# Kernel tuning notes

Hardware: AMD Instinct MI355X
Metric: run time of the kernel (lower is better)

The kernel has to match this reference:

```python
import jax, jax.numpy as jnp
import numpy as np

B, C, H, W = 4, 64, 256, 256
HEADS, WS = 2, 8
HID = int(C * 2.66)  # 170


def _layernorm(x, w, b):
    # Restormer per-pixel channel LayerNorm over C of BCHW, biased var, eps=1e-5
    mu = x.mean(axis=1, keepdims=True)
    var = x.var(axis=1, keepdims=True)
    xn = (x - mu) / jnp.sqrt(var + 1e-5)
    return xn * w[None, :, None, None] + b[None, :, None, None]


def _conv1x1(x, w, b=None):
    y = jnp.einsum('oc,bchw->bohw', w, x)
    if b is not None:
        y = y + b[None, :, None, None]
    return y


def _dwconv3(x, w):
    # depthwise 3x3, zero padding ('zeros' padding_mode)
    return jax.lax.conv_general_dilated(
        x, w, window_strides=(1, 1), padding='SAME',
        dimension_numbers=('NCHW', 'OIHW', 'NCHW'),
        feature_group_count=x.shape[1])


def _l2norm(x, eps=1e-12):
    n = jnp.sqrt(jnp.sum(x * x, axis=-1, keepdims=True))
    return x / jnp.maximum(n, eps)


def _attention(xn, qkv_w, qkv_dw_w, temperature, proj_w, proj_b):
    qkv = _dwconv3(_conv1x1(xn, qkv_w), qkv_dw_w)  # [B, 3C, H, W]
    h1, w1 = H // WS, W // WS
    c = C // HEADS
    # 'b (z head c) (h1 h) (w1 w) -> z (b h1 w1) head c (h w)'
    t = qkv.reshape(B, 3, HEADS, c, h1, WS, w1, WS)
    t = t.transpose(1, 0, 4, 6, 2, 3, 5, 7).reshape(3, B * h1 * w1, HEADS, c, WS * WS)
    q, k, v = t[0], t[1], t[2]
    q = _l2norm(q)
    k = _l2norm(k)
    attn = jnp.einsum('nhcd,nhed->nhce', q, k) * temperature  # [n, heads, c, c]
    attn = jax.nn.softmax(attn, axis=-1)
    out = jnp.einsum('nhce,nhed->nhcd', attn, v)
    # '(b h1 w1) head c (h w) -> b (head c) (h1 h) (w1 w)'
    out = out.reshape(B, h1, w1, HEADS, c, WS, WS)
    out = out.transpose(0, 3, 4, 1, 5, 2, 6).reshape(B, C, H, W)
    return _conv1x1(out, proj_w, proj_b)


def _ffn(xn, pin_w, dw_w, pout_w):
    y = _dwconv3(_conv1x1(xn, pin_w), dw_w)  # [B, 2*HID, H, W]
    y1, y2 = y[:, :HID], y[:, HID:]
    y = jax.nn.gelu(y1, approximate=False) * y2
    return _conv1x1(y, pout_w)


def setup_inputs() -> dict:
    key = jax.random.key(0)
    ks = jax.random.split(key, 8)
    s = 0.02
    return {
        'x': jax.random.normal(ks[0], (B, C, H, W), jnp.float32),
        'ln1_w': jnp.ones((C,), jnp.float32),
        'ln1_b': jnp.zeros((C,), jnp.float32),
        'qkv_w': jax.random.normal(ks[1], (3 * C, C), jnp.float32) * s,
        'qkv_dw_w': jax.random.normal(ks[2], (3 * C, 1, 3, 3), jnp.float32) * s,
        'temperature': jnp.ones((HEADS, 1, 1), jnp.float32) / np.float32(np.sqrt(C)),
        'proj_w': jax.random.normal(ks[3], (C, C), jnp.float32) * s,
        'proj_b': jnp.zeros((C,), jnp.float32),
        'ln2_w': jnp.ones((C,), jnp.float32),
        'ln2_b': jnp.zeros((C,), jnp.float32),
        'pin_w': jax.random.normal(ks[4], (2 * HID, C), jnp.float32) * s,
        'dw_w': jax.random.normal(ks[5], (2 * HID, 1, 3, 3), jnp.float32) * s,
        'pout_w': jax.random.normal(ks[6], (C, HID), jnp.float32) * s,
    }


def reference(x, ln1_w, ln1_b, qkv_w, qkv_dw_w, temperature, proj_w, proj_b,
              ln2_w, ln2_b, pin_w, dw_w, pout_w):
    x = x + _attention(_layernorm(x, ln1_w, ln1_b), qkv_w, qkv_dw_w,
                       temperature, proj_w, proj_b)
    x = x + _ffn(_layernorm(x, ln2_w, ln2_b), pin_w, dw_w, pout_w)
    return x
```

## Files before the change

kernel.cpp:

```cpp
#include <hip/hip_runtime.h>
#include <math.h>

typedef __attribute__((ext_vector_type(8))) short short8;
typedef __attribute__((ext_vector_type(4))) float f32x4;

#define HID 170
#define PLANE 65536

__device__ __forceinline__ unsigned short f2bf(float f) {
  unsigned u = __float_as_uint(f);
  u += 0x7FFFu + ((u >> 16) & 1u);
  return (unsigned short)(u >> 16);
}
__device__ __forceinline__ float bf2f(unsigned short h) {
  return __uint_as_float(((unsigned)h) << 16);
}
__device__ __forceinline__ float bf2f_lo(unsigned v) { return __uint_as_float(v << 16); }
__device__ __forceinline__ float bf2f_hi(unsigned v) { return __uint_as_float(v & 0xFFFF0000u); }
__device__ __forceinline__ unsigned pack2bf(float a, float b) {
  return (unsigned)f2bf(a) | ((unsigned)f2bf(b) << 16);
}
__device__ __forceinline__ f32x4 mfma16(short8 a, short8 b, f32x4 c) {
  return __builtin_amdgcn_mfma_f32_16x16x32_bf16(a, b, c, 0, 0, 0);
}

__global__ void prepack_kernel(const float* __restrict__ qkv_w, const float* __restrict__ proj_w,
                               const float* __restrict__ pin_w, const float* __restrict__ pout_w,
                               short* __restrict__ pq, short* __restrict__ pp,
                               short* __restrict__ pi, short* __restrict__ po) {
  int idx = blockIdx.x * 256 + threadIdx.x;
  if (idx < 12288) {
    int j = idx & 7, ln = (idx >> 3) & 63, ks = (idx >> 9) & 1, mt = idx >> 10;
    int row = mt * 16 + (ln & 15), k = ks * 32 + (ln >> 4) * 8 + j;
    pq[idx] = (short)f2bf(qkv_w[row * 64 + k]);
  }
  if (idx < 4096) {
    int j = idx & 7, ln = (idx >> 3) & 63, ks = (idx >> 9) & 1, mt = idx >> 10;
    int row = mt * 16 + (ln & 15), k = ks * 32 + (ln >> 4) * 8 + j;
    pp[idx] = (short)f2bf(proj_w[row * 64 + k]);
  }
  if (idx < 22528) {
    int j = idx & 7, ln = (idx >> 3) & 63, ks = (idx >> 9) & 1, mt = idx >> 10;
    int r = mt * 16 + (ln & 15), k = ks * 32 + (ln >> 4) * 8 + j;
    int c = r >> 7; if (c > 2) c = 2;
    int loc = r - c * 128;
    int half = (c < 2) ? 64 : 48, limit = (c < 2) ? 64 : 42;
    float v = 0.f;
    if (loc < half) { int i = loc; if (i < limit) v = pin_w[(c * 64 + i) * 64 + k]; }
    else { int i = loc - half; if (i < limit) v = pin_w[(HID + c * 64 + i) * 64 + k]; }
    pi[idx] = (short)f2bf(v);
  }
  if (idx < 12288) {
    int j = idx & 7, ln = (idx >> 3) & 63, ks = (idx >> 9) % 6, mt = idx / 3072;
    int o = mt * 16 + (ln & 15), k = ks * 32 + (ln >> 4) * 8 + j;
    float v = (k < 170) ? pout_w[o * 170 + k] : 0.f;
    po[idx] = (short)f2bf(v);
  }
}

__global__ __launch_bounds__(256) void ln_kernel(
    const float* __restrict__ src, const float* __restrict__ w,
    const float* __restrict__ bia, unsigned short* __restrict__ dst) {
  __shared__ float xT[64 * 65];
  const int t = threadIdx.x;
  const int g = blockIdx.x << 6;
  const int bi = g >> 16;
  const int hw = g & 65535;
  {
    int c = t >> 2, q = t & 3;
    const float* sp = src + ((size_t)(bi * 64 + c) << 16) + hw + q * 16;
    float4 v0 = *(const float4*)(sp);
    float4 v1 = *(const float4*)(sp + 4);
    float4 v2 = *(const float4*)(sp + 8);
    float4 v3 = *(const float4*)(sp + 12);
    float* row = xT + c * 65 + q * 16;
    row[0] = v0.x; row[1] = v0.y; row[2] = v0.z; row[3] = v0.w;
    row[4] = v1.x; row[5] = v1.y; row[6] = v1.z; row[7] = v1.w;
    row[8] = v2.x; row[9] = v2.y; row[10] = v2.z; row[11] = v2.w;
    row[12] = v3.x; row[13] = v3.y; row[14] = v3.z; row[15] = v3.w;
  }
  __syncthreads();
  const int p = t >> 2, q = t & 3;
  float s = 0.f, s2 = 0.f;
  float vv[16];
#pragma unroll
  for (int i = 0; i < 16; ++i) {
    float v = xT[(q * 16 + i) * 65 + p];
    vv[i] = v; s += v; s2 += v * v;
  }
  s += __shfl_xor(s, 1); s2 += __shfl_xor(s2, 1);
  s += __shfl_xor(s, 2); s2 += __shfl_xor(s2, 2);
  float mu = s * (1.f / 64.f);
  float var = s2 * (1.f / 64.f) - mu * mu;
  float rstd = rsqrtf(var + 1e-5f);
  short8 o0, o1;
#pragma unroll
  for (int i = 0; i < 8; ++i) {
    o0[i] = (short)f2bf((vv[i] - mu) * rstd * w[q * 16 + i] + bia[q * 16 + i]);
    o1[i] = (short)f2bf((vv[8 + i] - mu) * rstd * w[q * 16 + 8 + i] + bia[q * 16 + 8 + i]);
  }
  unsigned short* dp = dst + (size_t)(g + p) * 64 + q * 16;
  *(short8*)dp = o0;
  *(short8*)(dp + 8) = o1;
}

#define A_QK    0
#define A_VT    18432
#define A_XN    27648
#define A_QKVT  41984
#define A_SCL   41984
#define A_PP    42496
#define A_PB    50944
#define A_OW    56064
#define A_TOT   65280

__global__ __launch_bounds__(512) void attn_kernel(
    const unsigned short* __restrict__ xn1, const float* __restrict__ x,
    const float* __restrict__ qkv_dw, const float* __restrict__ temp,
    const float* __restrict__ proj_b,
    const short* __restrict__ pk_qkv, const short* __restrict__ pk_proj,
    float* __restrict__ x1out) {
  __shared__ __align__(16) char smem[A_TOT];
  short* qk      = (short*)(smem + A_QK);
  short* vt      = (short*)(smem + A_VT);
  short* xn      = (short*)(smem + A_XN);
  unsigned* qkvt = (unsigned*)(smem + A_QKVT);
  float* scl     = (float*)(smem + A_SCL);
  float* pP      = (float*)(smem + A_PP);
  short* pB      = (short*)(smem + A_PB);
  short* ow      = (short*)(smem + A_OW);

  const int tid = threadIdx.x;
  const int lane = tid & 63;
  const int wid = tid >> 6;
  const int l15 = lane & 15, q4 = lane >> 4;
  const int blk = blockIdx.x;
  const int b = blk >> 10, wy = (blk >> 5) & 31, wx = blk & 31;
  const int gy0 = wy * 8 - 1, gx0 = wx * 8 - 1;
  const size_t nb = (size_t)b << 16;

  for (int u = tid; u < 896; u += 512) {
    int p = u >> 3, q = u & 7;
    short8 v = {0, 0, 0, 0, 0, 0, 0, 0};
    if (p < 100) {
      int py = p / 10, px = p - py * 10;
      int gy = gy0 + py, gx = gx0 + px;
      if ((unsigned)gy < 256u && (unsigned)gx < 256u)
        v = *(const short8*)(xn1 + ((nb + gy * 256 + gx) << 6) + q * 8);
    }
    *(short8*)(xn + p * 64 + ((q ^ (p & 7)) << 3)) = v;
  }
  __syncthreads();

  for (int cc = 0; cc < 2; ++cc) {
    for (int f = wid; f < 42; f += 8) {
      int mt = f / 7, nt = f - mt * 7;
      int gmt = cc * 6 + mt;
      f32x4 acc = {0.f, 0.f, 0.f, 0.f};
#pragma unroll
      for (int ks = 0; ks < 2; ++ks) {
        short8 a = *(const short8*)(pk_qkv + ((gmt * 2 + ks) * 64 + lane) * 8);
        int pos0 = nt * 16 + l15;
        short8 bb = *(const short8*)(xn + pos0 * 64 + (((ks * 4 + q4) ^ (pos0 & 7)) << 3));
        acc = mfma16(a, bb, acc);
      }
      int pos = nt * 16 + l15;
      if (pos < 100) {
        int pb = mt * 8 + q4 * 2;
        qkvt[pb * 102 + pos]       = pack2bf(acc[0], acc[1]);
        qkvt[(pb + 1) * 102 + pos] = pack2bf(acc[2], acc[3]);
      }
    }
    __syncthreads();
    if (tid < 384) {
      int p = tid >> 3, r = tid & 7;
      int gp = cc * 48 + p;
      const float* w0 = qkv_dw + gp * 18;
      const float* w1 = w0 + 9;
      const unsigned* src = qkvt + p * 102;
      float accA[8], accB[8];
#pragma unroll
      for (int j = 0; j < 8; ++j) { accA[j] = 0.f; accB[j] = 0.f; }
#pragma unroll
      for (int t = 0; t < 3; ++t) {
        const unsigned* rp = src + (r + t) * 10;
        uint2 u0 = *(const uint2*)(rp);
        uint2 u1 = *(const uint2*)(rp + 2);
        uint2 u2 = *(const uint2*)(rp + 4);
        uint2 u3 = *(const uint2*)(rp + 6);
        uint2 u4 = *(const uint2*)(rp + 8);
        float lo[10], hi[10];
        lo[0] = bf2f_lo(u0.x); hi[0] = bf2f_hi(u0.x);
        lo[1] = bf2f_lo(u0.y); hi[1] = bf2f_hi(u0.y);
        lo[2] = bf2f_lo(u1.x); hi[2] = bf2f_hi(u1.x);
        lo[3] = bf2f_lo(u1.y); hi[3] = bf2f_hi(u1.y);
        lo[4] = bf2f_lo(u2.x); hi[4] = bf2f_hi(u2.x);
        lo[5] = bf2f_lo(u2.y); hi[5] = bf2f_hi(u2.y);
        lo[6] = bf2f_lo(u3.x); hi[6] = bf2f_hi(u3.x);
        lo[7] = bf2f_lo(u3.y); hi[7] = bf2f_hi(u3.y);
        lo[8] = bf2f_lo(u4.x); hi[8] = bf2f_hi(u4.x);
        lo[9] = bf2f_lo(u4.y); hi[9] = bf2f_hi(u4.y);
        float wa0 = w0[t * 3], wa1 = w0[t * 3 + 1], wa2 = w0[t * 3 + 2];
        float wb0 = w1[t * 3], wb1 = w1[t * 3 + 1], wb2 = w1[t * 3 + 2];
#pragma unroll
        for (int px = 0; px < 8; ++px) {
          accA[px] = fmaf(wa0, lo[px], fmaf(wa1, lo[px + 1], fmaf(wa2, lo[px + 2], accA[px])));
          accB[px] = fmaf(wb0, hi[px], fmaf(wb1, hi[px + 1], fmaf(wb2, hi[px + 2], accB[px])));
        }
      }
      if (gp < 64) {
        short8 sa, sb;
#pragma unroll
        for (int j = 0; j < 8; ++j) { sa[j] = (short)f2bf(accA[j]); sb[j] = (short)f2bf(accB[j]); }
        *(short8*)(qk + (2 * gp) * 72 + r * 8) = sa;
        *(short8*)(qk + (2 * gp + 1) * 72 + r * 8) = sb;
      } else {
        int vb = (gp - 64) * 2;
#pragma unroll
        for (int px = 0; px < 8; ++px)
          *(unsigned*)(vt + (r * 8 + px) * 72 + vb) = pack2bf(accA[px], accB[px]);
      }
    }
    __syncthreads();
  }

  {
    int row = tid >> 2, qq = tid & 3;
    const short* r = qk + row * 72 + qq * 16;
    short8 v0 = *(const short8*)(r);
    short8 v1 = *(const short8*)(r + 8);
    float s = 0.f;
#pragma unroll
    for (int j = 0; j < 8; ++j) {
      float f0 = bf2f((unsigned short)v0[j]); s = fmaf(f0, f0, s);
      float f1 = bf2f((unsigned short)v1[j]); s = fmaf(f1, f1, s);
    }
    s += __shfl_xor(s, 1);
    s += __shfl_xor(s, 2);
    if (qq == 0) scl[row] = 1.f / fmaxf(sqrtf(s), 1e-12f);
  }
  __syncthreads();

  {
    int h = wid >> 2, mt = (wid >> 1) & 1, nt = wid & 1;
    int arow = h * 32 + mt * 16;
    int brow = 64 + h * 32 + nt * 16;
    f32x4 acc = {0.f, 0.f, 0.f, 0.f};
#pragma unroll
    for (int ks = 0; ks < 2; ++ks) {
      short8 a = *(const short8*)(qk + (arow + l15) * 72 + ks * 32 + q4 * 8);
      short8 bb = *(const short8*)(qk + (brow + l15) * 72 + ks * 32 + q4 * 8);
      acc = mfma16(a, bb, acc);
    }
    float tf = temp[h];
    int e = nt * 16 + l15;
    float se = scl[64 + h * 32 + e] * tf;
    int cqb = h * 32 + mt * 16 + q4 * 4;
#pragma unroll
    for (int j = 0; j < 4; ++j)
      pP[(cqb + j) * 33 + e] = acc[j] * scl[cqb + j] * se;
  }
  __syncthreads();

  {
    int row = tid >> 3, l = tid & 7;
    const float* rp = pP + row * 33 + l * 4;
    float e0 = rp[0], e1 = rp[1], e2 = rp[2], e3 = rp[3];
    float m = fmaxf(fmaxf(e0, e1), fmaxf(e2, e3));
    m = fmaxf(m, __shfl_xor(m, 1));
    m = fmaxf(m, __shfl_xor(m, 2));
    m = fmaxf(m, __shfl_xor(m, 4));
    float x0 = __expf(e0 - m), x1v = __expf(e1 - m);
    float x2 = __expf(e2 - m), x3 = __expf(e3 - m);
    float s = x0 + x1v + x2 + x3;
    s += __shfl_xor(s, 1);
    s += __shfl_xor(s, 2);
    s += __shfl_xor(s, 4);
    float inv = 1.f / s;
    unsigned* dp = (unsigned*)(pB + row * 40 + l * 4);
    dp[0] = pack2bf(x0 * inv, x1v * inv);
    dp[1] = pack2bf(x2 * inv, x3 * inv);
  }
  __syncthreads();

#pragma unroll
  for (int r = 0; r < 2; ++r) {
    int f = wid + r * 8;
    int h = f >> 3, mt = (f >> 2) & 1, nt = f & 3;
    short8 a = *(const short8*)(pB + (h * 32 + mt * 16 + l15) * 40 + q4 * 8);
    short8 bb = *(const short8*)(vt + (nt * 16 + l15) * 72 + h * 32 + q4 * 8);
    f32x4 acc = {0.f, 0.f, 0.f, 0.f};
    acc = mfma16(a, bb, acc);
    int d = nt * 16 + l15;
    int chb = h * 32 + mt * 16 + q4 * 4;
    unsigned* dp = (unsigned*)(ow + d * 72 + chb);
    dp[0] = pack2bf(acc[0], acc[1]);
    dp[1] = pack2bf(acc[2], acc[3]);
  }
  __syncthreads();

#pragma unroll
  for (int r = 0; r < 2; ++r) {
    int f = wid + r * 8;
    int mt = f >> 2, nt = f & 3;
    f32x4 acc = {0.f, 0.f, 0.f, 0.f};
#pragma unroll
    for (int ks = 0; ks < 2; ++ks) {
      short8 a = *(const short8*)(pk_proj + ((mt * 2 + ks) * 64 + lane) * 8);
      short8 bb = *(const short8*)(ow + (nt * 16 + l15) * 72 + ks * 32 + q4 * 8);
      acc = mfma16(a, bb, acc);
    }
    int pos = nt * 16 + l15;
    int gy = wy * 8 + (pos >> 3), gx = wx * 8 + (pos & 7);
    int ob = mt * 16 + q4 * 4;
#pragma unroll
    for (int j = 0; j < 4; ++j) {
      int o = ob + j;
      size_t gp = (size_t)(b * 64 + o) * PLANE + gy * 256 + gx;
      x1out[gp] = acc[j] + proj_b[o] + x[gp];
    }
  }
}

#define F_XN  0
#define F_Y12 14336
#define F_G   40448
#define F_TOT 49664

__global__ __launch_bounds__(512) void ffn_kernel(
    const unsigned short* __restrict__ xn2,
    const float* __restrict__ dw_w,
    const short* __restrict__ pk_pin, const short* __restrict__ pk_pout,
    float* __restrict__ out) {
  __shared__ __align__(16) char smem[F_TOT];
  short* xn      = (short*)(smem + F_XN);
  unsigned* y12  = (unsigned*)(smem + F_Y12);
  short* y12s    = (short*)(smem + F_Y12);
  short* g       = (short*)(smem + F_G);

  const int tid = threadIdx.x;
  const int lane = tid & 63;
  const int wid = tid >> 6;
  const int l15 = lane & 15, q4 = lane >> 4;
  const int blk = blockIdx.x;
  const int b = blk >> 10, wy = (blk >> 5) & 31, wx = blk & 31;
  const int gy0 = wy * 8 - 1, gx0 = wx * 8 - 1;
  const size_t nb = (size_t)b << 16;

  for (int u = tid; u < 896; u += 512) {
    int p = u >> 3, q = u & 7;
    short8 v = {0, 0, 0, 0, 0, 0, 0, 0};
    if (p < 100) {
      int py = p / 10, px = p - py * 10;
      int gy = gy0 + py, gx = gx0 + px;
      if ((unsigned)gy < 256u && (unsigned)gx < 256u)
        v = *(const short8*)(xn2 + ((nb + gy * 256 + gx) << 6) + q * 8);
    }
    *(short8*)(xn + p * 64 + ((q ^ (p & 7)) << 3)) = v;
  }
  __syncthreads();

  f32x4 acc0 = {0.f, 0.f, 0.f, 0.f}, acc1 = {0.f, 0.f, 0.f, 0.f};

  for (int cc2 = 0; cc2 < 3; ++cc2) {
    const int MT = (cc2 < 2) ? 8 : 6;
    const int YM = (cc2 < 2) ? 4 : 3;
    const int mbase = cc2 * 8;
    for (int f = wid; f < MT * 7; f += 8) {
      int lm = f / 7, nt = f - lm * 7;
      int gmt = mbase + lm;
      f32x4 acc = {0.f, 0.f, 0.f, 0.f};
#pragma unroll
      for (int ks = 0; ks < 2; ++ks) {
        short8 a = *(const short8*)(pk_pin + ((gmt * 2 + ks) * 64 + lane) * 8);
        int pos0 = nt * 16 + l15;
        short8 bb = *(const short8*)(xn + pos0 * 64 + (((ks * 4 + q4) ^ (pos0 & 7)) << 3));
        acc = mfma16(a, bb, acc);
      }
      int pos = nt * 16 + l15;
      if (pos < 100) {
        int isY = lm < YM;
        int i0 = (isY ? lm : lm - YM) * 16 + q4 * 4;
        int half = isY ? 0 : 1;
#pragma unroll
        for (int j = 0; j < 4; ++j)
          y12s[((i0 + j) * 102 + pos) * 2 + half] = (short)f2bf(acc[j]);
      }
    }
    __syncthreads();
    {
      int nv = (cc2 < 2) ? 64 : 42;
      int p = tid >> 3, r = tid & 7;
      if (p < nv) {
        const float* wY = dw_w + (cc2 * 64 + p) * 9;
        const float* wZ = dw_w + (HID + cc2 * 64 + p) * 9;
        const unsigned* src = y12 + p * 102;
        float accA[8], accB[8];
#pragma unroll
        for (int j = 0; j < 8; ++j) { accA[j] = 0.f; accB[j] = 0.f; }
#pragma unroll
        for (int t = 0; t < 3; ++t) {
          const unsigned* rp = src + (r + t) * 10;
          uint2 u0 = *(const uint2*)(rp);
          uint2 u1 = *(const uint2*)(rp + 2);
          uint2 u2 = *(const uint2*)(rp + 4);
          uint2 u3 = *(const uint2*)(rp + 6);
          uint2 u4 = *(const uint2*)(rp + 8);
          float lo[10], hi[10];
          lo[0] = bf2f_lo(u0.x); hi[0] = bf2f_hi(u0.x);
          lo[1] = bf2f_lo(u0.y); hi[1] = bf2f_hi(u0.y);
          lo[2] = bf2f_lo(u1.x); hi[2] = bf2f_hi(u1.x);
          lo[3] = bf2f_lo(u1.y); hi[3] = bf2f_hi(u1.y);
          lo[4] = bf2f_lo(u2.x); hi[4] = bf2f_hi(u2.x);
          lo[5] = bf2f_lo(u2.y); hi[5] = bf2f_hi(u2.y);
          lo[6] = bf2f_lo(u3.x); hi[6] = bf2f_hi(u3.x);
          lo[7] = bf2f_lo(u3.y); hi[7] = bf2f_hi(u3.y);
          lo[8] = bf2f_lo(u4.x); hi[8] = bf2f_hi(u4.x);
          lo[9] = bf2f_lo(u4.y); hi[9] = bf2f_hi(u4.y);
          float wa0 = wY[t * 3], wa1 = wY[t * 3 + 1], wa2 = wY[t * 3 + 2];
          float wb0 = wZ[t * 3], wb1 = wZ[t * 3 + 1], wb2 = wZ[t * 3 + 2];
#pragma unroll
          for (int px = 0; px < 8; ++px) {
            accA[px] = fmaf(wa0, lo[px], fmaf(wa1, lo[px + 1], fmaf(wa2, lo[px + 2], accA[px])));
            accB[px] = fmaf(wb0, hi[px], fmaf(wb1, hi[px + 1], fmaf(wb2, hi[px + 2], accB[px])));
          }
        }
#pragma unroll
        for (int px = 0; px < 8; ++px) {
          float y = accA[px];
          float u2 = -2.f * y * fmaf(0.0356774081f, y * y, 0.7978845608f);
          float ge = y / (1.f + __expf(u2));
          g[(r * 8 + px) * 72 + p] = (short)f2bf(ge * accB[px]);
        }
      }
    }
    __syncthreads();
    {
      int mt0 = wid >> 2, nt = wid & 3;
      int mt1 = mt0 + 2;
#pragma unroll
      for (int ks = 0; ks < 2; ++ks) {
        int gks = cc2 * 2 + ks;
        short8 bb = *(const short8*)(g + (nt * 16 + l15) * 72 + ks * 32 + q4 * 8);
        short8 a0 = *(const short8*)(pk_pout + ((mt0 * 6 + gks) * 64 + lane) * 8);
        short8 a1 = *(const short8*)(pk_pout + ((mt1 * 6 + gks) * 64 + lane) * 8);
        acc0 = mfma16(a0, bb, acc0);
        acc1 = mfma16(a1, bb, acc1);
      }
    }
    __syncthreads();
  }

  {
    int mt0 = wid >> 2, nt = wid & 3;
    int pos = nt * 16 + l15;
    int gy = wy * 8 + (pos >> 3), gx = wx * 8 + (pos & 7);
#pragma unroll
    for (int r = 0; r < 2; ++r) {
      f32x4 acc = r ? acc1 : acc0;
      int mt = r ? (mt0 + 2) : mt0;
      int ob = mt * 16 + q4 * 4;
#pragma unroll
      for (int j = 0; j < 4; ++j) {
        int o = ob + j;
        size_t gp = (size_t)(b * 64 + o) * PLANE + gy * 256 + gx;
        out[gp] = acc[j] + out[gp];
      }
    }
  }
}

extern "C" void kernel_launch(void* const* d_in, const int* in_sizes, int n_in,
                              void* d_out, int out_size, void* d_ws, size_t ws_size,
                              hipStream_t stream) {
  const float* x      = (const float*)d_in[0];
  const float* ln1_w  = (const float*)d_in[1];
  const float* ln1_b  = (const float*)d_in[2];
  const float* qkv_w  = (const float*)d_in[3];
  const float* qkv_dw = (const float*)d_in[4];
  const float* temp   = (const float*)d_in[5];
  const float* proj_w = (const float*)d_in[6];
  const float* proj_b = (const float*)d_in[7];
  const float* ln2_w  = (const float*)d_in[8];
  const float* ln2_b  = (const float*)d_in[9];
  const float* pin_w  = (const float*)d_in[10];
  const float* dw_w   = (const float*)d_in[11];
  const float* pout_w = (const float*)d_in[12];
  float* out = (float*)d_out;

  unsigned short* xnbuf = (unsigned short*)d_ws;
  short* pq = (short*)((char*)d_ws + 33554432);
  short* pp = pq + 12288;
  short* pi = pp + 4096;
  short* po = pi + 22528;

  prepack_kernel<<<dim3(88), dim3(256), 0, stream>>>(qkv_w, proj_w, pin_w, pout_w, pq, pp, pi, po);
  ln_kernel<<<dim3(4096), dim3(256), 0, stream>>>(x, ln1_w, ln1_b, xnbuf);
  attn_kernel<<<dim3(4096), dim3(512), 0, stream>>>(xnbuf, x, qkv_dw, temp, proj_b, pq, pp, out);
  ln_kernel<<<dim3(4096), dim3(256), 0, stream>>>(out, ln2_w, ln2_b, xnbuf);
  ffn_kernel<<<dim3(4096), dim3(512), 0, stream>>>(xnbuf, dw_w, pi, po, out);
}
```

Measured before the change: 449.5 us.

## Fuse LayerNorm into pointwise GEMMs and run per-batch pipeline with halo-free GEMM

Moves the LayerNorm into new GEMM kernels that compute the 1x1 qkv and pin projections once per pixel and store bf16 results to a workspace. The attention and FFN kernels then load the precomputed projections with halos instead of recomputing the 1x1 GEMM over a 10x10 halo tile per 8x8 window. The launch is split into four per-batch passes so the intermediate buffer stays small and may stay cache-resident. The FFN output projection now runs once after all channel chunks, using a wider g buffer. In exchange there is extra global traffic for the intermediates, more kernel launches, and redundant halo loads.

```diff
diff --git a/kernel.cpp b/kernel.cpp
--- a/kernel.cpp
+++ b/kernel.cpp
@@ -22,6 +22,12 @@
 }
 __device__ __forceinline__ f32x4 mfma16(short8 a, short8 b, f32x4 c) {
   return __builtin_amdgcn_mfma_f32_16x16x32_bf16(a, b, c, 0, 0, 0);
+}
+__device__ __forceinline__ uint2 pack4bf(f32x4 v) {
+  uint2 r;
+  r.x = pack2bf(v[0], v[1]);
+  r.y = pack2bf(v[2], v[3]);
+  return r;
 }
 
 __global__ void prepack_kernel(const float* __restrict__ qkv_w, const float* __restrict__ proj_w,
@@ -41,135 +47,198 @@
   }
   if (idx < 22528) {
     int j = idx & 7, ln = (idx >> 3) & 63, ks = (idx >> 9) & 1, mt = idx >> 10;
-    int r = mt * 16 + (ln & 15), k = ks * 32 + (ln >> 4) * 8 + j;
-    int c = r >> 7; if (c > 2) c = 2;
-    int loc = r - c * 128;
-    int half = (c < 2) ? 64 : 48, limit = (c < 2) ? 64 : 42;
+    int r = mt * 16 + (ln & 15);
+    int k = ks * 32 + (ln >> 4) * 8 + j;
+    int i = r >> 1, half = r & 1;
     float v = 0.f;
-    if (loc < half) { int i = loc; if (i < limit) v = pin_w[(c * 64 + i) * 64 + k]; }
-    else { int i = loc - half; if (i < limit) v = pin_w[(HID + c * 64 + i) * 64 + k]; }
+    if (i < HID) v = pin_w[(half ? HID + i : i) * 64 + k];
     pi[idx] = (short)f2bf(v);
   }
   if (idx < 12288) {
     int j = idx & 7, ln = (idx >> 3) & 63, ks = (idx >> 9) % 6, mt = idx / 3072;
     int o = mt * 16 + (ln & 15), k = ks * 32 + (ln >> 4) * 8 + j;
-    float v = (k < 170) ? pout_w[o * 170 + k] : 0.f;
+    float v = (k < HID) ? pout_w[o * HID + k] : 0.f;
     po[idx] = (short)f2bf(v);
   }
 }
 
-__global__ __launch_bounds__(256) void ln_kernel(
-    const float* __restrict__ src, const float* __restrict__ w,
-    const float* __restrict__ bia, unsigned short* __restrict__ dst) {
-  __shared__ float xT[64 * 65];
+__global__ __launch_bounds__(256) void gemm_qkv(
+    const float* __restrict__ src, const float* __restrict__ lnw,
+    const float* __restrict__ lnb, const short* __restrict__ pq,
+    unsigned short* __restrict__ y1) {
+  __shared__ __align__(16) char smem[24832];
+  short* xn = (short*)smem;
+  float* xT = (float*)(smem + 8192);
   const int t = threadIdx.x;
-  const int g = blockIdx.x << 6;
-  const int bi = g >> 16;
-  const int hw = g & 65535;
+  const int posbase = blockIdx.x << 6;
   {
     int c = t >> 2, q = t & 3;
-    const float* sp = src + ((size_t)(bi * 64 + c) << 16) + hw + q * 16;
+    const float* sp = src + ((size_t)c << 16) + posbase + q * 16;
     float4 v0 = *(const float4*)(sp);
     float4 v1 = *(const float4*)(sp + 4);
     float4 v2 = *(const float4*)(sp + 8);
     float4 v3 = *(const float4*)(sp + 12);
     float* row = xT + c * 65 + q * 16;
-    row[0] = v0.x; row[1] = v0.y; row[2] = v0.z; row[3] = v0.w;
-    row[4] = v1.x; row[5] = v1.y; row[6] = v1.z; row[7] = v1.w;
-    row[8] = v2.x; row[9] = v2.y; row[10] = v2.z; row[11] = v2.w;
-    row[12] = v3.x; row[13] = v3.y; row[14] = v3.z; row[15] = v3.w;
-  }
-  __syncthreads();
-  const int p = t >> 2, q = t & 3;
-  float s = 0.f, s2 = 0.f;
-  float vv[16];
-#pragma unroll
-  for (int i = 0; i < 16; ++i) {
-    float v = xT[(q * 16 + i) * 65 + p];
-    vv[i] = v; s += v; s2 += v * v;
-  }
-  s += __shfl_xor(s, 1); s2 += __shfl_xor(s2, 1);
-  s += __shfl_xor(s, 2); s2 += __shfl_xor(s2, 2);
-  float mu = s * (1.f / 64.f);
-  float var = s2 * (1.f / 64.f) - mu * mu;
-  float rstd = rsqrtf(var + 1e-5f);
-  short8 o0, o1;
-#pragma unroll
-  for (int i = 0; i < 8; ++i) {
-    o0[i] = (short)f2bf((vv[i] - mu) * rstd * w[q * 16 + i] + bia[q * 16 + i]);
-    o1[i] = (short)f2bf((vv[8 + i] - mu) * rstd * w[q * 16 + 8 + i] + bia[q * 16 + 8 + i]);
-  }
-  unsigned short* dp = dst + (size_t)(g + p) * 64 + q * 16;
-  *(short8*)dp = o0;
-  *(short8*)(dp + 8) = o1;
-}
-
-#define A_QK    0
-#define A_VT    18432
-#define A_XN    27648
-#define A_QKVT  41984
-#define A_SCL   41984
-#define A_PP    42496
-#define A_PB    50944
-#define A_OW    56064
-#define A_TOT   65280
-
-__global__ __launch_bounds__(512) void attn_kernel(
-    const unsigned short* __restrict__ xn1, const float* __restrict__ x,
+    row[0]=v0.x; row[1]=v0.y; row[2]=v0.z; row[3]=v0.w;
+    row[4]=v1.x; row[5]=v1.y; row[6]=v1.z; row[7]=v1.w;
+    row[8]=v2.x; row[9]=v2.y; row[10]=v2.z; row[11]=v2.w;
+    row[12]=v3.x; row[13]=v3.y; row[14]=v3.z; row[15]=v3.w;
+  }
+  __syncthreads();
+  {
+    int p = t >> 2, q = t & 3;
+    float s = 0.f, s2 = 0.f;
+    float vv[16];
+#pragma unroll
+    for (int i = 0; i < 16; ++i) {
+      float v = xT[(q * 16 + i) * 65 + p];
+      vv[i] = v; s += v; s2 += v * v;
+    }
+    s += __shfl_xor(s, 1); s2 += __shfl_xor(s2, 1);
+    s += __shfl_xor(s, 2); s2 += __shfl_xor(s2, 2);
+    float mu = s * (1.f / 64.f);
+    float var = s2 * (1.f / 64.f) - mu * mu;
+    float rstd = rsqrtf(var + 1e-5f);
+    short8 o0, o1;
+#pragma unroll
+    for (int i = 0; i < 8; ++i) {
+      o0[i] = (short)f2bf((vv[i] - mu) * rstd * lnw[q * 16 + i] + lnb[q * 16 + i]);
+      o1[i] = (short)f2bf((vv[8 + i] - mu) * rstd * lnw[q * 16 + 8 + i] + lnb[q * 16 + 8 + i]);
+    }
+    *(short8*)(xn + p * 64 + (((2 * q) ^ (p & 7)) << 3)) = o0;
+    *(short8*)(xn + p * 64 + (((2 * q + 1) ^ (p & 7)) << 3)) = o1;
+  }
+  __syncthreads();
+  const int lane = t & 63, wid = t >> 6;
+  const int l15 = lane & 15, q4 = lane >> 4;
+#pragma unroll
+  for (int m = 0; m < 3; ++m) {
+    int mt = wid * 3 + m;
+    short8 a0 = *(const short8*)(pq + ((mt * 2 + 0) * 64 + lane) * 8);
+    short8 a1 = *(const short8*)(pq + ((mt * 2 + 1) * 64 + lane) * 8);
+#pragma unroll
+    for (int nt = 0; nt < 4; ++nt) {
+      int pos = nt * 16 + l15;
+      short8 b0 = *(const short8*)(xn + pos * 64 + (((q4) ^ (pos & 7)) << 3));
+      short8 b1 = *(const short8*)(xn + pos * 64 + (((4 + q4) ^ (pos & 7)) << 3));
+      f32x4 acc = {0.f, 0.f, 0.f, 0.f};
+      acc = mfma16(a0, b0, acc);
+      acc = mfma16(a1, b1, acc);
+      *(uint2*)(y1 + (size_t)(posbase + pos) * 192 + mt * 16 + q4 * 4) = pack4bf(acc);
+    }
+  }
+}
+
+__global__ __launch_bounds__(256) void gemm_pin(
+    const float* __restrict__ src, const float* __restrict__ lnw,
+    const float* __restrict__ lnb, const short* __restrict__ pi,
+    unsigned short* __restrict__ y2) {
+  __shared__ __align__(16) char smem[24832];
+  short* xn = (short*)smem;
+  float* xT = (float*)(smem + 8192);
+  const int t = threadIdx.x;
+  const int posbase = blockIdx.x << 6;
+  {
+    int c = t >> 2, q = t & 3;
+    const float* sp = src + ((size_t)c << 16) + posbase + q * 16;
+    float4 v0 = *(const float4*)(sp);
+    float4 v1 = *(const float4*)(sp + 4);
+    float4 v2 = *(const float4*)(sp + 8);
+    float4 v3 = *(const float4*)(sp + 12);
+    float* row = xT + c * 65 + q * 16;
+    row[0]=v0.x; row[1]=v0.y; row[2]=v0.z; row[3]=v0.w;
+    row[4]=v1.x; row[5]=v1.y; row[6]=v1.z; row[7]=v1.w;
+    row[8]=v2.x; row[9]=v2.y; row[10]=v2.z; row[11]=v2.w;
+    row[12]=v3.x; row[13]=v3.y; row[14]=v3.z; row[15]=v3.w;
+  }
+  __syncthreads();
+  {
+    int p = t >> 2, q = t & 3;
+    float s = 0.f, s2 = 0.f;
+    float vv[16];
+#pragma unroll
+    for (int i = 0; i < 16; ++i) {
+      float v = xT[(q * 16 + i) * 65 + p];
+      vv[i] = v; s += v; s2 += v * v;
+    }
+    s += __shfl_xor(s, 1); s2 += __shfl_xor(s2, 1);
+    s += __shfl_xor(s, 2); s2 += __shfl_xor(s2, 2);
+    float mu = s * (1.f / 64.f);
+    float var = s2 * (1.f / 64.f) - mu * mu;
+    float rstd = rsqrtf(var + 1e-5f);
+    short8 o0, o1;
+#pragma unroll
+    for (int i = 0; i < 8; ++i) {
+      o0[i] = (short)f2bf((vv[i] - mu) * rstd * lnw[q * 16 + i] + lnb[q * 16 + i]);
+      o1[i] = (short)f2bf((vv[8 + i] - mu) * rstd * lnw[q * 16 + 8 + i] + lnb[q * 16 + 8 + i]);
+    }
+    *(short8*)(xn + p * 64 + (((2 * q) ^ (p & 7)) << 3)) = o0;
+    *(short8*)(xn + p * 64 + (((2 * q + 1) ^ (p & 7)) << 3)) = o1;
+  }
+  __syncthreads();
+  const int lane = t & 63, wid = t >> 6;
+  const int l15 = lane & 15, q4 = lane >> 4;
+#pragma unroll
+  for (int m = 0; m < 6; ++m) {
+    int mt = m * 4 + wid;
+    if (mt < 22) {
+      short8 a0 = *(const short8*)(pi + ((mt * 2 + 0) * 64 + lane) * 8);
+      short8 a1 = *(const short8*)(pi + ((mt * 2 + 1) * 64 + lane) * 8);
+#pragma unroll
+      for (int nt = 0; nt < 4; ++nt) {
+        int pos = nt * 16 + l15;
+        short8 b0 = *(const short8*)(xn + pos * 64 + (((q4) ^ (pos & 7)) << 3));
+        short8 b1 = *(const short8*)(xn + pos * 64 + (((4 + q4) ^ (pos & 7)) << 3));
+        f32x4 acc = {0.f, 0.f, 0.f, 0.f};
+        acc = mfma16(a0, b0, acc);
+        acc = mfma16(a1, b1, acc);
+        *(uint2*)(y2 + (size_t)(posbase + pos) * 352 + mt * 16 + q4 * 4) = pack4bf(acc);
+      }
+    }
+  }
+}
+
+#define A2_QKVT 0
+#define A2_QK   19584
+#define A2_VT   38016
+#define A2_SCL  47232
+#define A2_PP   0
+#define A2_PB   8448
+#define A2_OW   19584
+#define A2_TOT  47744
+
+__global__ __launch_bounds__(512) void attn2_kernel(
+    const unsigned short* __restrict__ y1, const float* __restrict__ x,
     const float* __restrict__ qkv_dw, const float* __restrict__ temp,
-    const float* __restrict__ proj_b,
-    const short* __restrict__ pk_qkv, const short* __restrict__ pk_proj,
+    const float* __restrict__ proj_b, const short* __restrict__ pk_proj,
     float* __restrict__ x1out) {
-  __shared__ __align__(16) char smem[A_TOT];
-  short* qk      = (short*)(smem + A_QK);
-  short* vt      = (short*)(smem + A_VT);
-  short* xn      = (short*)(smem + A_XN);
-  unsigned* qkvt = (unsigned*)(smem + A_QKVT);
-  float* scl     = (float*)(smem + A_SCL);
-  float* pP      = (float*)(smem + A_PP);
-  short* pB      = (short*)(smem + A_PB);
-  short* ow      = (short*)(smem + A_OW);
+  __shared__ __align__(16) char smem[A2_TOT];
+  unsigned* qkvt = (unsigned*)(smem + A2_QKVT);
+  short* qk  = (short*)(smem + A2_QK);
+  short* vt  = (short*)(smem + A2_VT);
+  float* scl = (float*)(smem + A2_SCL);
+  float* pP  = (float*)(smem + A2_PP);
+  short* pB  = (short*)(smem + A2_PB);
+  short* ow  = (short*)(smem + A2_OW);
+  const unsigned* y1d = (const unsigned*)y1;
 
   const int tid = threadIdx.x;
   const int lane = tid & 63;
   const int wid = tid >> 6;
   const int l15 = lane & 15, q4 = lane >> 4;
   const int blk = blockIdx.x;
-  const int b = blk >> 10, wy = (blk >> 5) & 31, wx = blk & 31;
+  const int wy = blk >> 5, wx = blk & 31;
   const int gy0 = wy * 8 - 1, gx0 = wx * 8 - 1;
-  const size_t nb = (size_t)b << 16;
-
-  for (int u = tid; u < 896; u += 512) {
-    int p = u >> 3, q = u & 7;
-    short8 v = {0, 0, 0, 0, 0, 0, 0, 0};
-    if (p < 100) {
+
+  for (int cc = 0; cc < 2; ++cc) {
+    for (int u = tid; u < 4800; u += 512) {
+      int p = u / 48, pr = u % 48;
       int py = p / 10, px = p - py * 10;
       int gy = gy0 + py, gx = gx0 + px;
+      unsigned v = 0;
       if ((unsigned)gy < 256u && (unsigned)gx < 256u)
-        v = *(const short8*)(xn1 + ((nb + gy * 256 + gx) << 6) + q * 8);
-    }
-    *(short8*)(xn + p * 64 + ((q ^ (p & 7)) << 3)) = v;
-  }
-  __syncthreads();
-
-  for (int cc = 0; cc < 2; ++cc) {
-    for (int f = wid; f < 42; f += 8) {
-      int mt = f / 7, nt = f - mt * 7;
-      int gmt = cc * 6 + mt;
-      f32x4 acc = {0.f, 0.f, 0.f, 0.f};
-#pragma unroll
-      for (int ks = 0; ks < 2; ++ks) {
-        short8 a = *(const short8*)(pk_qkv + ((gmt * 2 + ks) * 64 + lane) * 8);
-        int pos0 = nt * 16 + l15;
-        short8 bb = *(const short8*)(xn + pos0 * 64 + (((ks * 4 + q4) ^ (pos0 & 7)) << 3));
-        acc = mfma16(a, bb, acc);
-      }
-      int pos = nt * 16 + l15;
-      if (pos < 100) {
-        int pb = mt * 8 + q4 * 2;
-        qkvt[pb * 102 + pos]       = pack2bf(acc[0], acc[1]);
-        qkvt[(pb + 1) * 102 + pos] = pack2bf(acc[2], acc[3]);
-      }
+        v = y1d[(size_t)(gy * 256 + gx) * 96 + cc * 48 + pr];
+      qkvt[pr * 102 + p] = v;
     }
     __syncthreads();
     if (tid < 384) {
@@ -190,28 +259,28 @@
         uint2 u3 = *(const uint2*)(rp + 6);
         uint2 u4 = *(const uint2*)(rp + 8);
         float lo[10], hi[10];
-        lo[0] = bf2f_lo(u0.x); hi[0] = bf2f_hi(u0.x);
-        lo[1] = bf2f_lo(u0.y); hi[1] = bf2f_hi(u0.y);
-        lo[2] = bf2f_lo(u1.x); hi[2] = bf2f_hi(u1.x);
-        lo[3] = bf2f_lo(u1.y); hi[3] = bf2f_hi(u1.y);
-        lo[4] = bf2f_lo(u2.x); hi[4] = bf2f_hi(u2.x);
-        lo[5] = bf2f_lo(u2.y); hi[5] = bf2f_hi(u2.y);
-        lo[6] = bf2f_lo(u3.x); hi[6] = bf2f_hi(u3.x);
-        lo[7] = bf2f_lo(u3.y); hi[7] = bf2f_hi(u3.y);
-        lo[8] = bf2f_lo(u4.x); hi[8] = bf2f_hi(u4.x);
-        lo[9] = bf2f_lo(u4.y); hi[9] = bf2f_hi(u4.y);
-        float wa0 = w0[t * 3], wa1 = w0[t * 3 + 1], wa2 = w0[t * 3 + 2];
-        float wb0 = w1[t * 3], wb1 = w1[t * 3 + 1], wb2 = w1[t * 3 + 2];
+        lo[0]=bf2f_lo(u0.x); hi[0]=bf2f_hi(u0.x);
+        lo[1]=bf2f_lo(u0.y); hi[1]=bf2f_hi(u0.y);
+        lo[2]=bf2f_lo(u1.x); hi[2]=bf2f_hi(u1.x);
+        lo[3]=bf2f_lo(u1.y); hi[3]=bf2f_hi(u1.y);
+        lo[4]=bf2f_lo(u2.x); hi[4]=bf2f_hi(u2.x);
+        lo[5]=bf2f_lo(u2.y); hi[5]=bf2f_hi(u2.y);
+        lo[6]=bf2f_lo(u3.x); hi[6]=bf2f_hi(u3.x);
+        lo[7]=bf2f_lo(u3.y); hi[7]=bf2f_hi(u3.y);
+        lo[8]=bf2f_lo(u4.x); hi[8]=bf2f_hi(u4.x);
+        lo[9]=bf2f_lo(u4.y); hi[9]=bf2f_hi(u4.y);
+        float wa0=w0[t*3], wa1=w0[t*3+1], wa2=w0[t*3+2];
+        float wb0=w1[t*3], wb1=w1[t*3+1], wb2=w1[t*3+2];
 #pragma unroll
         for (int px = 0; px < 8; ++px) {
-          accA[px] = fmaf(wa0, lo[px], fmaf(wa1, lo[px + 1], fmaf(wa2, lo[px + 2], accA[px])));
-          accB[px] = fmaf(wb0, hi[px], fmaf(wb1, hi[px + 1], fmaf(wb2, hi[px + 2], accB[px])));
+          accA[px] = fmaf(wa0, lo[px], fmaf(wa1, lo[px+1], fmaf(wa2, lo[px+2], accA[px])));
+          accB[px] = fmaf(wb0, hi[px], fmaf(wb1, hi[px+1], fmaf(wb2, hi[px+2], accB[px])));
         }
       }
       if (gp < 64) {
         short8 sa, sb;
 #pragma unroll
-        for (int j = 0; j < 8; ++j) { sa[j] = (short)f2bf(accA[j]); sb[j] = (short)f2bf(accB[j]); }
+        for (int j = 0; j < 8; ++j) { sa[j]=(short)f2bf(accA[j]); sb[j]=(short)f2bf(accB[j]); }
         *(short8*)(qk + (2 * gp) * 72 + r * 8) = sa;
         *(short8*)(qk + (2 * gp + 1) * 72 + r * 8) = sb;
       } else {
@@ -316,84 +385,57 @@
 #pragma unroll
     for (int j = 0; j < 4; ++j) {
       int o = ob + j;
-      size_t gp = (size_t)(b * 64 + o) * PLANE + gy * 256 + gx;
+      size_t gp = (size_t)o * PLANE + gy * 256 + gx;
       x1out[gp] = acc[j] + proj_b[o] + x[gp];
     }
   }
 }
 
-#define F_XN  0
-#define F_Y12 14336
-#define F_G   40448
-#define F_TOT 49664
-
-__global__ __launch_bounds__(512) void ffn_kernel(
-    const unsigned short* __restrict__ xn2,
-    const float* __restrict__ dw_w,
-    const short* __restrict__ pk_pin, const short* __restrict__ pk_pout,
+#define F2_Y12 0
+#define F2_G   26112
+#define F2_TOT 51712
+
+__global__ __launch_bounds__(512) void ffn2_kernel(
+    const unsigned short* __restrict__ y2,
+    const float* __restrict__ dw_w, const short* __restrict__ pk_pout,
     float* __restrict__ out) {
-  __shared__ __align__(16) char smem[F_TOT];
-  short* xn      = (short*)(smem + F_XN);
-  unsigned* y12  = (unsigned*)(smem + F_Y12);
-  short* y12s    = (short*)(smem + F_Y12);
-  short* g       = (short*)(smem + F_G);
+  __shared__ __align__(16) char smem[F2_TOT];
+  unsigned* y12 = (unsigned*)(smem + F2_Y12);
+  short* g      = (short*)(smem + F2_G);
+  const unsigned* y2d = (const unsigned*)y2;
 
   const int tid = threadIdx.x;
   const int lane = tid & 63;
   const int wid = tid >> 6;
   const int l15 = lane & 15, q4 = lane >> 4;
   const int blk = blockIdx.x;
-  const int b = blk >> 10, wy = (blk >> 5) & 31, wx = blk & 31;
+  const int wy = blk >> 5, wx = blk & 31;
   const int gy0 = wy * 8 - 1, gx0 = wx * 8 - 1;
-  const size_t nb = (size_t)b << 16;
-
-  for (int u = tid; u < 896; u += 512) {
-    int p = u >> 3, q = u & 7;
-    short8 v = {0, 0, 0, 0, 0, 0, 0, 0};
-    if (p < 100) {
+
+  for (int u = tid; u < 704; u += 512) {
+    int pos = u / 11, k = u - pos * 11;
+    ((unsigned*)g)[pos * 100 + 85 + k] = 0;
+  }
+
+  for (int c = 0; c < 3; ++c) {
+    for (int u = tid; u < 6400; u += 512) {
+      int p = u >> 6, pr = u & 63;
       int py = p / 10, px = p - py * 10;
       int gy = gy0 + py, gx = gx0 + px;
-      if ((unsigned)gy < 256u && (unsigned)gx < 256u)
-        v = *(const short8*)(xn2 + ((nb + gy * 256 + gx) << 6) + q * 8);
-    }
-    *(short8*)(xn + p * 64 + ((q ^ (p & 7)) << 3)) = v;
-  }
-  __syncthreads();
-
-  f32x4 acc0 = {0.f, 0.f, 0.f, 0.f}, acc1 = {0.f, 0.f, 0.f, 0.f};
-
-  for (int cc2 = 0; cc2 < 3; ++cc2) {
-    const int MT = (cc2 < 2) ? 8 : 6;
-    const int YM = (cc2 < 2) ? 4 : 3;
-    const int mbase = cc2 * 8;
-    for (int f = wid; f < MT * 7; f += 8) {
-      int lm = f / 7, nt = f - lm * 7;
-      int gmt = mbase + lm;
-      f32x4 acc = {0.f, 0.f, 0.f, 0.f};
-#pragma unroll
-      for (int ks = 0; ks < 2; ++ks) {
-        short8 a = *(const short8*)(pk_pin + ((gmt * 2 + ks) * 64 + lane) * 8);
-        int pos0 = nt * 16 + l15;
-        short8 bb = *(const short8*)(xn + pos0 * 64 + (((ks * 4 + q4) ^ (pos0 & 7)) << 3));
-        acc = mfma16(a, bb, acc);
-      }
-      int pos = nt * 16 + l15;
-      if (pos < 100) {
-        int isY = lm < YM;
-        int i0 = (isY ? lm : lm - YM) * 16 + q4 * 4;
-        int half = isY ? 0 : 1;
-#pragma unroll
-        for (int j = 0; j < 4; ++j)
-          y12s[((i0 + j) * 102 + pos) * 2 + half] = (short)f2bf(acc[j]);
-      }
+      int gpair = c * 64 + pr;
+      unsigned v = 0;
+      if ((unsigned)gy < 256u && (unsigned)gx < 256u && gpair < 176)
+        v = y2d[(size_t)(gy * 256 + gx) * 176 + gpair];
+      y12[pr * 102 + p] = v;
     }
     __syncthreads();
     {
-      int nv = (cc2 < 2) ? 64 : 42;
+      int nv = (c < 2) ? 64 : 42;
       int p = tid >> 3, r = tid & 7;
       if (p < nv) {
-        const float* wY = dw_w + (cc2 * 64 + p) * 9;
-        const float* wZ = dw_w + (HID + cc2 * 64 + p) * 9;
+        int gp = c * 64 + p;
+        const float* wY = dw_w + gp * 9;
+        const float* wZ = dw_w + (HID + gp) * 9;
         const unsigned* src = y12 + p * 102;
         float accA[8], accB[8];
 #pragma unroll
@@ -407,63 +449,59 @@
           uint2 u3 = *(const uint2*)(rp + 6);
           uint2 u4 = *(const uint2*)(rp + 8);
           float lo[10], hi[10];
-          lo[0] = bf2f_lo(u0.x); hi[0] = bf2f_hi(u0.x);
-          lo[1] = bf2f_lo(u0.y); hi[1] = bf2f_hi(u0.y);
-          lo[2] = bf2f_lo(u1.x); hi[2] = bf2f_hi(u1.x);
-          lo[3] = bf2f_lo(u1.y); hi[3] = bf2f_hi(u1.y);
-          lo[4] = bf2f_lo(u2.x); hi[4] = bf2f_hi(u2.x);
-          lo[5] = bf2f_lo(u2.y); hi[5] = bf2f_hi(u2.y);
-          lo[6] = bf2f_lo(u3.x); hi[6] = bf2f_hi(u3.x);
-          lo[7] = bf2f_lo(u3.y); hi[7] = bf2f_hi(u3.y);
-          lo[8] = bf2f_lo(u4.x); hi[8] = bf2f_hi(u4.x);
-          lo[9] = bf2f_lo(u4.y); hi[9] = bf2f_hi(u4.y);
-          float wa0 = wY[t * 3], wa1 = wY[t * 3 + 1], wa2 = wY[t * 3 + 2];
-          float wb0 = wZ[t * 3], wb1 = wZ[t * 3 + 1], wb2 = wZ[t * 3 + 2];
+          lo[0]=bf2f_lo(u0.x); hi[0]=bf2f_hi(u0.x);
+          lo[1]=bf2f_lo(u0.y); hi[1]=bf2f_hi(u0.y);
+          lo[2]=bf2f_lo(u1.x); hi[2]=bf2f_hi(u1.x);
+          lo[3]=bf2f_lo(u1.y); hi[3]=bf2f_hi(u1.y);
+          lo[4]=bf2f_lo(u2.x); hi[4]=bf2f_hi(u2.x);
+          lo[5]=bf2f_lo(u2.y); hi[5]=bf2f_hi(u2.y);
+          lo[6]=bf2f_lo(u3.x); hi[6]=bf2f_hi(u3.x);
+          lo[7]=bf2f_lo(u3.y); hi[7]=bf2f_hi(u3.y);
+          lo[8]=bf2f_lo(u4.x); hi[8]=bf2f_hi(u4.x);
+          lo[9]=bf2f_lo(u4.y); hi[9]=bf2f_hi(u4.y);
+          float wa0=wY[t*3], wa1=wY[t*3+1], wa2=wY[t*3+2];
+          float wb0=wZ[t*3], wb1=wZ[t*3+1], wb2=wZ[t*3+2];
 #pragma unroll
           for (int px = 0; px < 8; ++px) {
-            accA[px] = fmaf(wa0, lo[px], fmaf(wa1, lo[px + 1], fmaf(wa2, lo[px + 2], accA[px])));
-            accB[px] = fmaf(wb0, hi[px], fmaf(wb1, hi[px + 1], fmaf(wb2, hi[px + 2], accB[px])));
+            accA[px] = fmaf(wa0, lo[px], fmaf(wa1, lo[px+1], fmaf(wa2, lo[px+2], accA[px])));
+            accB[px] = fmaf(wb0, hi[px], fmaf(wb1, hi[px+1], fmaf(wb2, hi[px+2], accB[px])));
           }
         }
 #pragma unroll
         for (int px = 0; px < 8; ++px) {
           float y = accA[px];
-          float u2 = -2.f * y * fmaf(0.0356774081f, y * y, 0.7978845608f);
-          float ge = y / (1.f + __expf(u2));
-          g[(r * 8 + px) * 72 + p] = (short)f2bf(ge * accB[px]);
+          float u2m = -2.f * y * fmaf(0.0356774081f, y * y, 0.7978845608f);
+          float ge = y / (1.f + __expf(u2m));
+          g[(r * 8 + px) * 200 + gp] = (short)f2bf(ge * accB[px]);
         }
       }
     }
     __syncthreads();
-    {
-      int mt0 = wid >> 2, nt = wid & 3;
-      int mt1 = mt0 + 2;
-#pragma unroll
-      for (int ks = 0; ks < 2; ++ks) {
-        int gks = cc2 * 2 + ks;
-        short8 bb = *(const short8*)(g + (nt * 16 + l15) * 72 + ks * 32 + q4 * 8);
-        short8 a0 = *(const short8*)(pk_pout + ((mt0 * 6 + gks) * 64 + lane) * 8);
-        short8 a1 = *(const short8*)(pk_pout + ((mt1 * 6 + gks) * 64 + lane) * 8);
-        acc0 = mfma16(a0, bb, acc0);
-        acc1 = mfma16(a1, bb, acc1);
-      }
-    }
-    __syncthreads();
   }
 
   {
     int mt0 = wid >> 2, nt = wid & 3;
+    int mt1 = mt0 + 2;
+    f32x4 acc0 = {0.f, 0.f, 0.f, 0.f}, acc1 = {0.f, 0.f, 0.f, 0.f};
+#pragma unroll
+    for (int ks = 0; ks < 6; ++ks) {
+      short8 bb = *(const short8*)(g + (nt * 16 + l15) * 200 + ks * 32 + q4 * 8);
+      short8 a0 = *(const short8*)(pk_pout + ((mt0 * 6 + ks) * 64 + lane) * 8);
+      short8 a1 = *(const short8*)(pk_pout + ((mt1 * 6 + ks) * 64 + lane) * 8);
+      acc0 = mfma16(a0, bb, acc0);
+      acc1 = mfma16(a1, bb, acc1);
+    }
     int pos = nt * 16 + l15;
     int gy = wy * 8 + (pos >> 3), gx = wx * 8 + (pos & 7);
 #pragma unroll
     for (int r = 0; r < 2; ++r) {
       f32x4 acc = r ? acc1 : acc0;
-      int mt = r ? (mt0 + 2) : mt0;
+      int mt = r ? mt1 : mt0;
       int ob = mt * 16 + q4 * 4;
 #pragma unroll
       for (int j = 0; j < 4; ++j) {
         int o = ob + j;
-        size_t gp = (size_t)(b * 64 + o) * PLANE + gy * 256 + gx;
+        size_t gp = (size_t)o * PLANE + gy * 256 + gx;
         out[gp] = acc[j] + out[gp];
       }
     }
@@ -488,15 +526,19 @@
   const float* pout_w = (const float*)d_in[12];
   float* out = (float*)d_out;
 
-  unsigned short* xnbuf = (unsigned short*)d_ws;
-  short* pq = (short*)((char*)d_ws + 33554432);
+  unsigned short* ybuf = (unsigned short*)d_ws;
+  short* pq = (short*)((char*)d_ws + 50331648);
   short* pp = pq + 12288;
   short* pi = pp + 4096;
   short* po = pi + 22528;
 
   prepack_kernel<<<dim3(88), dim3(256), 0, stream>>>(qkv_w, proj_w, pin_w, pout_w, pq, pp, pi, po);
-  ln_kernel<<<dim3(4096), dim3(256), 0, stream>>>(x, ln1_w, ln1_b, xnbuf);
-  attn_kernel<<<dim3(4096), dim3(512), 0, stream>>>(xnbuf, x, qkv_dw, temp, proj_b, pq, pp, out);
-  ln_kernel<<<dim3(4096), dim3(256), 0, stream>>>(out, ln2_w, ln2_b, xnbuf);
-  ffn_kernel<<<dim3(4096), dim3(512), 0, stream>>>(xnbuf, dw_w, pi, po, out);
-}
+
+  for (int q = 0; q < 4; ++q) {
+    size_t qoff = (size_t)q * 64 * PLANE;
+    gemm_qkv<<<dim3(1024), dim3(256), 0, stream>>>(x + qoff, ln1_w, ln1_b, pq, ybuf);
+    attn2_kernel<<<dim3(1024), dim3(512), 0, stream>>>(ybuf, x + qoff, qkv_dw, temp, proj_b, pp, out + qoff);
+    gemm_pin<<<dim3(1024), dim3(256), 0, stream>>>(out + qoff, ln2_w, ln2_b, pi, ybuf);
+    ffn2_kernel<<<dim3(1024), dim3(512), 0, stream>>>(ybuf, dw_w, po, out + qoff);
+  }
+}
```

Measured after the change: 598.4 us. 1.33x slower.
